# Kernel tuning notes

Measured on AMD Instinct MI355X. Metric: run time of the kernel, lower is better.

Reference implementation:

```python
import jax, jax.numpy as jnp
import numpy as np

B, N, E, D = 16, 100000, 10, 3


def setup_inputs() -> dict:
    key = jax.random.key(0)
    k1, k2, k3, k4 = jax.random.split(key, 4)
    coord1 = jax.random.normal(k1, (B, N, D), dtype=jnp.float32)
    coord2 = jax.random.normal(k2, (B, N, D), dtype=jnp.float32)
    base = jax.random.randint(k3, (B, N, E), 0, N, dtype=jnp.int64)
    drop = jax.random.uniform(k4, (B, N, E)) < 0.25
    drop = drop.at[:, :, 0].set(False)
    A_list = jnp.where(drop, jnp.int64(-1), base)
    return {"coord1": coord1, "coord2": coord2, "A_list": A_list}


def _centroid(coord, A_list):
    # coord: [B,N,D], A_list: [B,N,E] with -1 for invalid slots
    valid = A_list >= 0                               # [B,N,E]
    idx = jnp.where(valid, A_list, 0)                 # clamp invalid to 0
    # vertices[b,n,e,:] = coord[b, idx[b,n,e], :]
    vertices = jax.vmap(lambda c, i: c[i])(coord, idx)  # [B,N,E,D]
    sum_nb = jnp.sum(vertices * valid[..., None].astype(coord.dtype), axis=2)  # [B,N,D]
    num_nb = jnp.sum(valid.astype(coord.dtype), axis=2, keepdims=True)         # [B,N,1]
    return sum_nb / num_nb


def reference(coord1, coord2, A_list):
    lap1 = coord1 - _centroid(coord1, A_list)
    lap2 = coord2 - _centroid(coord2, A_list)
    # MSELoss(reduction='mean') * num_points
    loss = jnp.mean((lap2 - lap1) ** 2) * coord1.shape[1]
    return loss
```

## Files before the change

kernel.cpp:

```cpp
#include <hip/hip_runtime.h>

constexpr int B = 16;
constexpr int N = 100000;
constexpr int E = 10;
constexpr int D = 3;

typedef float        f32x4 __attribute__((ext_vector_type(4)));
typedef unsigned int u32x2 __attribute__((ext_vector_type(2)));
typedef unsigned int u32x4 __attribute__((ext_vector_type(4)));

__device__ __forceinline__ unsigned int bf16_rne(float f) {
    unsigned int u = __float_as_uint(f);
    u += 0x7fffu + ((u >> 16) & 1u);
    return u >> 16;
}
__device__ __forceinline__ float bf16_lo(unsigned int w) {
    return __uint_as_float(w << 16);
}
__device__ __forceinline__ float bf16_hi(unsigned int w) {
    return __uint_as_float(w & 0xffff0000u);
}

__global__ __launch_bounds__(256) void diff_bf16_kernel(const float* __restrict__ c1,
                                                        const float* __restrict__ c2,
                                                        unsigned int* __restrict__ outp,
                                                        int nquad) {
    int per = gridDim.x >> 3;
    int w = (blockIdx.x & 7) * per + (blockIdx.x >> 3);
    int i = w * blockDim.x + threadIdx.x;
    if (i >= nquad) return;
    const f32x4* a4 = reinterpret_cast<const f32x4*>(c1) + (size_t)i * 3;
    const f32x4* b4 = reinterpret_cast<const f32x4*>(c2) + (size_t)i * 3;
    f32x4 a0 = __builtin_nontemporal_load(a4 + 0);
    f32x4 a1 = __builtin_nontemporal_load(a4 + 1);
    f32x4 a2 = __builtin_nontemporal_load(a4 + 2);
    f32x4 b0 = __builtin_nontemporal_load(b4 + 0);
    f32x4 b1 = __builtin_nontemporal_load(b4 + 1);
    f32x4 b2 = __builtin_nontemporal_load(b4 + 2);
    float d[12];
    d[0] = b0.x - a0.x; d[1] = b0.y - a0.y; d[2]  = b0.z - a0.z; d[3]  = b0.w - a0.w;
    d[4] = b1.x - a1.x; d[5] = b1.y - a1.y; d[6]  = b1.z - a1.z; d[7]  = b1.w - a1.w;
    d[8] = b2.x - a2.x; d[9] = b2.y - a2.y; d[10] = b2.z - a2.z; d[11] = b2.w - a2.w;

    u32x4 o0, o1;
    o0.x = bf16_rne(d[0]) | (bf16_rne(d[1]) << 16);
    o0.y = bf16_rne(d[2]);
    o0.z = bf16_rne(d[3]) | (bf16_rne(d[4]) << 16);
    o0.w = bf16_rne(d[5]);
    o1.x = bf16_rne(d[6]) | (bf16_rne(d[7]) << 16);
    o1.y = bf16_rne(d[8]);
    o1.z = bf16_rne(d[9]) | (bf16_rne(d[10]) << 16);
    o1.w = bf16_rne(d[11]);

    u32x4* o = reinterpret_cast<u32x4*>(outp) + (size_t)i * 2;
    o[0] = o0;
    o[1] = o1;
}

__global__ __launch_bounds__(256, 8) void loss_kernel(const unsigned int* __restrict__ diff,
                                                      const int* __restrict__ A,
                                                      float* __restrict__ out) {
    int per = gridDim.x >> 3;
    int w = (blockIdx.x & 7) * per + (blockIdx.x >> 3);
    int node = w * blockDim.x + threadIdx.x;

    float sq = 0.0f;
    if (node < B * N) {
        int b = node / N;
        const long long* ap = reinterpret_cast<const long long*>(A + (size_t)node * E);
        long long q0 = __builtin_nontemporal_load(ap + 0);
        long long q1 = __builtin_nontemporal_load(ap + 1);
        long long q2 = __builtin_nontemporal_load(ap + 2);
        long long q3 = __builtin_nontemporal_load(ap + 3);
        long long q4 = __builtin_nontemporal_load(ap + 4);
        int idx[E] = {(int)q0, (int)(q0 >> 32), (int)q1, (int)(q1 >> 32),
                      (int)q2, (int)(q2 >> 32), (int)q3, (int)(q3 >> 32),
                      (int)q4, (int)(q4 >> 32)};

        const u32x2* db = reinterpret_cast<const u32x2*>(diff) + (size_t)b * N;
        u32x2 v[E];
        float m[E];
        #pragma unroll
        for (int e = 0; e < E; ++e) {
            int ix = idx[e];
            m[e] = (ix >= 0) ? 1.0f : 0.0f;
            v[e] = db[ix >= 0 ? ix : 0];
        }
        u32x2 ov = db[node - b * N];

        float sx = 0.f, sy = 0.f, sz = 0.f, fcnt = 0.f;
        #pragma unroll
        for (int e = 0; e < E; ++e) {
            sx = fmaf(bf16_lo(v[e].x), m[e], sx);
            sy = fmaf(bf16_hi(v[e].x), m[e], sy);
            sz = fmaf(bf16_lo(v[e].y), m[e], sz);
            fcnt += m[e];
        }
        float inv = 1.0f / fcnt;
        float lx = bf16_lo(ov.x) - sx * inv;
        float ly = bf16_hi(ov.x) - sy * inv;
        float lz = bf16_lo(ov.y) - sz * inv;
        sq = lx * lx + ly * ly + lz * lz;
    }

    #pragma unroll
    for (int off = 32; off > 0; off >>= 1)
        sq += __shfl_down(sq, off, 64);

    __shared__ float wsum[4];
    int lane = threadIdx.x & 63;
    int wid = threadIdx.x >> 6;
    if (lane == 0) wsum[wid] = sq;
    __syncthreads();
    if (threadIdx.x == 0) {
        float t = (wsum[0] + wsum[1]) + (wsum[2] + wsum[3]);
        atomicAdd(out, t * (1.0f / (float)(B * D)));
    }
}

extern "C" void kernel_launch(void* const* d_in, const int* in_sizes, int n_in,
                              void* d_out, int out_size, void* d_ws, size_t ws_size,
                              hipStream_t stream) {
    const float* coord1 = (const float*)d_in[0];
    const float* coord2 = (const float*)d_in[1];
    const int* A_list = (const int*)d_in[2];
    float* out = (float*)d_out;
    unsigned int* diff = (unsigned int*)d_ws;

    hipMemsetAsync(out, 0, sizeof(float), stream);

    int nodes = B * N;
    int nquad = nodes / 4;
    int dblk = (nquad + 255) / 256;
    dblk = (dblk + 7) & ~7;
    diff_bf16_kernel<<<dblk, 256, 0, stream>>>(coord1, coord2, diff, nquad);

    int nblk = (nodes + 255) / 256;
    nblk = (nblk + 7) & ~7;
    loss_kernel<<<nblk, 256, 0, stream>>>(diff, A_list, out);
}
```

Measured before the change: 111.7 us.

## Stream per-batch diff table through LDS tiles instead of random global gathers

Replaces the one-thread-per-node gather kernel with a tiled kernel. Each 1024-thread block owns 4 nodes per thread from one batch and sweeps that batch's full bf16 diff table through a 64KB shared-memory tile, with register double-buffering of the next tile. Neighbour lookups are resolved by a range check against the current tile, so random global gathers become LDS reads. Each block now re-reads the whole 800KB batch table (32 blocks per batch) and runs 13 passes with branches per neighbour slot. The output memset is also folded into the first kernel, which removes one launch.

```diff
diff --git a/kernel.cpp b/kernel.cpp
--- a/kernel.cpp
+++ b/kernel.cpp
@@ -3,7 +3,6 @@
 constexpr int B = 16;
 constexpr int N = 100000;
 constexpr int E = 10;
-constexpr int D = 3;
 
 typedef float        f32x4 __attribute__((ext_vector_type(4)));
 typedef unsigned int u32x2 __attribute__((ext_vector_type(2)));
@@ -14,17 +13,15 @@
     u += 0x7fffu + ((u >> 16) & 1u);
     return u >> 16;
 }
-__device__ __forceinline__ float bf16_lo(unsigned int w) {
-    return __uint_as_float(w << 16);
-}
-__device__ __forceinline__ float bf16_hi(unsigned int w) {
-    return __uint_as_float(w & 0xffff0000u);
-}
+__device__ __forceinline__ float bf16_lo(unsigned int w) { return __uint_as_float(w << 16); }
+__device__ __forceinline__ float bf16_hi(unsigned int w) { return __uint_as_float(w & 0xffff0000u); }
 
 __global__ __launch_bounds__(256) void diff_bf16_kernel(const float* __restrict__ c1,
                                                         const float* __restrict__ c2,
                                                         unsigned int* __restrict__ outp,
+                                                        float* __restrict__ out,
                                                         int nquad) {
+    if (blockIdx.x == 0 && threadIdx.x == 0) *out = 0.0f;
     int per = gridDim.x >> 3;
     int w = (blockIdx.x & 7) * per + (blockIdx.x >> 3);
     int i = w * blockDim.x + threadIdx.x;
@@ -57,64 +54,122 @@
     o[1] = o1;
 }
 
-__global__ __launch_bounds__(256, 8) void loss_kernel(const unsigned int* __restrict__ diff,
-                                                      const int* __restrict__ A,
-                                                      float* __restrict__ out) {
-    int per = gridDim.x >> 3;
-    int w = (blockIdx.x & 7) * per + (blockIdx.x >> 3);
-    int node = w * blockDim.x + threadIdx.x;
+constexpr int TPB   = 1024;
+constexpr int SLOTS = 32;
+constexpr int NPB   = N / SLOTS;
+constexpr int NPT   = 4;
+constexpr int TILE  = 8192;
+constexpr int NPASS = (N + TILE - 1) / TILE;
+constexpr int SPT   = TILE / TPB;
+constexpr int LOSS_BLOCKS = B * SLOTS;
 
-    float sq = 0.0f;
-    if (node < B * N) {
-        int b = node / N;
+__global__ __launch_bounds__(TPB, 4) void loss_tiled(const unsigned int* __restrict__ diff,
+                                                     const int* __restrict__ A,
+                                                     float* __restrict__ out) {
+    __shared__ u32x2 tile[TILE];
+
+    const int g = blockIdx.x;
+    const int b = (g & 7) + 8 * ((g >> 3) & 1);
+    const int base = (g >> 4) * NPB;
+    const int t = threadIdx.x;
+    const u32x2 zv = {0u, 0u};
+
+    const u32x2* db = reinterpret_cast<const u32x2*>(diff) + (size_t)b * N;
+
+    int idx[NPT][E];
+    float cnt[NPT];
+    float sx[NPT], sy[NPT], sz[NPT];
+    #pragma unroll
+    for (int s = 0; s < NPT; ++s) {
+        sx[s] = sy[s] = sz[s] = 0.f;
+        int l = s * TPB + t;
+        bool a = (l < NPB);
+        int node = b * N + base + (a ? l : 0);
         const long long* ap = reinterpret_cast<const long long*>(A + (size_t)node * E);
         long long q0 = __builtin_nontemporal_load(ap + 0);
         long long q1 = __builtin_nontemporal_load(ap + 1);
         long long q2 = __builtin_nontemporal_load(ap + 2);
         long long q3 = __builtin_nontemporal_load(ap + 3);
         long long q4 = __builtin_nontemporal_load(ap + 4);
-        int idx[E] = {(int)q0, (int)(q0 >> 32), (int)q1, (int)(q1 >> 32),
-                      (int)q2, (int)(q2 >> 32), (int)q3, (int)(q3 >> 32),
-                      (int)q4, (int)(q4 >> 32)};
+        idx[s][0] = a ? (int)q0 : -1;  idx[s][1] = a ? (int)(q0 >> 32) : -1;
+        idx[s][2] = a ? (int)q1 : -1;  idx[s][3] = a ? (int)(q1 >> 32) : -1;
+        idx[s][4] = a ? (int)q2 : -1;  idx[s][5] = a ? (int)(q2 >> 32) : -1;
+        idx[s][6] = a ? (int)q3 : -1;  idx[s][7] = a ? (int)(q3 >> 32) : -1;
+        idx[s][8] = a ? (int)q4 : -1;  idx[s][9] = a ? (int)(q4 >> 32) : -1;
+        float c = 0.f;
+        #pragma unroll
+        for (int e = 0; e < E; ++e) c += (idx[s][e] >= 0) ? 1.f : 0.f;
+        cnt[s] = a ? c : 1.f;
+    }
 
-        const u32x2* db = reinterpret_cast<const u32x2*>(diff) + (size_t)b * N;
-        u32x2 v[E];
-        float m[E];
+    u32x2 stg[SPT];
+    #pragma unroll
+    for (int k = 0; k < SPT; ++k) {
+        int j = k * TPB + t;
+        stg[k] = (j < N) ? db[j] : zv;
+    }
+    #pragma unroll
+    for (int k = 0; k < SPT; ++k) tile[k * TPB + t] = stg[k];
+
+    #pragma unroll 1
+    for (int p = 0; p < NPASS; ++p) {
+        __syncthreads();
+        const int lo = p * TILE;
+        if (p + 1 < NPASS) {
+            const int lo2 = lo + TILE;
+            #pragma unroll
+            for (int k = 0; k < SPT; ++k) {
+                int j = lo2 + k * TPB + t;
+                stg[k] = (j < N) ? db[j] : zv;
+            }
+        }
         #pragma unroll
-        for (int e = 0; e < E; ++e) {
-            int ix = idx[e];
-            m[e] = (ix >= 0) ? 1.0f : 0.0f;
-            v[e] = db[ix >= 0 ? ix : 0];
+        for (int s = 0; s < NPT; ++s) {
+            #pragma unroll
+            for (int e = 0; e < E; ++e) {
+                unsigned r = (unsigned)(idx[s][e] - lo);
+                if (r < (unsigned)TILE) {
+                    u32x2 v = tile[r];
+                    sx[s] += bf16_lo(v.x);
+                    sy[s] += bf16_hi(v.x);
+                    sz[s] += bf16_lo(v.y);
+                }
+            }
         }
-        u32x2 ov = db[node - b * N];
+        __syncthreads();
+        if (p + 1 < NPASS) {
+            #pragma unroll
+            for (int k = 0; k < SPT; ++k) tile[k * TPB + t] = stg[k];
+        }
+    }
 
-        float sx = 0.f, sy = 0.f, sz = 0.f, fcnt = 0.f;
-        #pragma unroll
-        for (int e = 0; e < E; ++e) {
-            sx = fmaf(bf16_lo(v[e].x), m[e], sx);
-            sy = fmaf(bf16_hi(v[e].x), m[e], sy);
-            sz = fmaf(bf16_lo(v[e].y), m[e], sz);
-            fcnt += m[e];
-        }
-        float inv = 1.0f / fcnt;
-        float lx = bf16_lo(ov.x) - sx * inv;
-        float ly = bf16_hi(ov.x) - sy * inv;
-        float lz = bf16_lo(ov.y) - sz * inv;
-        sq = lx * lx + ly * ly + lz * lz;
+    float acc = 0.f;
+    #pragma unroll
+    for (int s = 0; s < NPT; ++s) {
+        int l = s * TPB + t;
+        bool a = (l < NPB);
+        u32x2 ov = db[base + (a ? l : 0)];
+        float inv = 1.0f / cnt[s];
+        float lx = bf16_lo(ov.x) - sx[s] * inv;
+        float ly = bf16_hi(ov.x) - sy[s] * inv;
+        float lz = bf16_lo(ov.y) - sz[s] * inv;
+        float sq = lx * lx + ly * ly + lz * lz;
+        acc += a ? sq : 0.f;
     }
 
     #pragma unroll
     for (int off = 32; off > 0; off >>= 1)
-        sq += __shfl_down(sq, off, 64);
+        acc += __shfl_down(acc, off, 64);
 
-    __shared__ float wsum[4];
-    int lane = threadIdx.x & 63;
-    int wid = threadIdx.x >> 6;
-    if (lane == 0) wsum[wid] = sq;
     __syncthreads();
-    if (threadIdx.x == 0) {
-        float t = (wsum[0] + wsum[1]) + (wsum[2] + wsum[3]);
-        atomicAdd(out, t * (1.0f / (float)(B * D)));
+    float* red = reinterpret_cast<float*>(tile);
+    if ((t & 63) == 0) red[t >> 6] = acc;
+    __syncthreads();
+    if (t == 0) {
+        float tot = 0.f;
+        #pragma unroll
+        for (int i = 0; i < TPB / 64; ++i) tot += red[i];
+        atomicAdd(out, tot * (1.0f / 48.0f));
     }
 }
 
@@ -127,15 +182,11 @@
     float* out = (float*)d_out;
     unsigned int* diff = (unsigned int*)d_ws;
 
-    hipMemsetAsync(out, 0, sizeof(float), stream);
-
     int nodes = B * N;
     int nquad = nodes / 4;
     int dblk = (nquad + 255) / 256;
     dblk = (dblk + 7) & ~7;
-    diff_bf16_kernel<<<dblk, 256, 0, stream>>>(coord1, coord2, diff, nquad);
+    diff_bf16_kernel<<<dblk, 256, 0, stream>>>(coord1, coord2, diff, out, nquad);
 
-    int nblk = (nodes + 255) / 256;
-    nblk = (nblk + 7) & ~7;
-    loss_kernel<<<nblk, 256, 0, stream>>>(diff, A_list, out);
+    loss_tiled<<<LOSS_BLOCKS, TPB, 0, stream>>>(diff, A_list, out);
 }
```

Result: slower. 133.7 us (+19.8%).
